# Performance work log

Hardware: AMD Instinct MI355X
Metric: run time of the kernel (lower is better)

The kernel has to match this reference:

```python
import jax, jax.numpy as jnp
import numpy as np

GRID_SIZE = 5
SPLINE_ORDER = 3
GRID_RANGE = (-1.0, 1.0)


def _make_grid():
    # knots: arange(-k, G+k+1)*h + lo, shared across in_features (uniform grid)
    h = (GRID_RANGE[1] - GRID_RANGE[0]) / GRID_SIZE
    return (jnp.arange(-SPLINE_ORDER, GRID_SIZE + SPLINE_ORDER + 1, dtype=jnp.float32) * h
            + GRID_RANGE[0])  # (G + 2k + 1,) = (12,)


def _b_splines(x2d, grid):
    # x2d: (T, C); grid: (12,) broadcast over features
    x = x2d[..., None]  # (T, C, 1)
    g = grid[None, None, :]  # (1, 1, 12)
    bases = ((x >= g[..., :-1]) & (x < g[..., 1:])).astype(x2d.dtype)
    for k in range(1, SPLINE_ORDER + 1):
        left = (x - g[..., : -(k + 1)]) / (g[..., k:-1] - g[..., : -(k + 1)])
        right = (g[..., k + 1:] - x) / (g[..., k + 1:] - g[..., 1:-k])
        bases = left * bases[..., :-1] + right * bases[..., 1:]
    return bases  # (T, C, G + k) = (T, C, 8)


def setup_inputs() -> dict:
    key = jax.random.key(0)
    k1, k2, k3, k4 = jax.random.split(key, 4)
    B, N, C, O = 4, 4096, 768, 768
    n_coef = GRID_SIZE + SPLINE_ORDER  # 8
    x = jax.random.normal(k1, (B, N, C), dtype=jnp.float32) * 0.5
    base_weight = jax.random.normal(k2, (O, C), dtype=jnp.float32) * (1.0 / np.sqrt(C))
    spline_weight = jax.random.normal(k3, (O, C, n_coef), dtype=jnp.float32) * 0.1
    spline_scaler = jax.random.normal(k4, (O, C), dtype=jnp.float32) * (1.0 / np.sqrt(C))
    return {"x": x, "base_weight": base_weight, "spline_weight": spline_weight,
            "spline_scaler": spline_scaler}


def reference(x, base_weight, spline_weight, spline_scaler):
    B, N, C = x.shape
    x2d = x.reshape(B * N, C)
    grid = _make_grid()
    # base path: SiLU activation + linear
    base_out = jnp.einsum('tc,oc->to', jax.nn.silu(x2d), base_weight)
    # spline path: B-spline bases + scaled linear combination
    bases = _b_splines(x2d, grid)  # (T, C, 8)
    w = spline_weight * spline_scaler[..., None]  # (O, C, 8)
    spline_out = jnp.einsum('tcg,ocg->to', bases, w)
    out = (base_out + spline_out).reshape(B, N, -1)
    return out  # dropout with p=0.0 is identity
```

## Files before the change

### kernel.cpp

```cpp
#include <hip/hip_runtime.h>

typedef __attribute__((ext_vector_type(8)))  short  short8;
typedef __attribute__((ext_vector_type(16))) float  f32x16;
typedef __attribute__((ext_vector_type(4)))  float  flt4;
typedef __attribute__((ext_vector_type(4)))  unsigned int u32x4;
typedef __attribute__((ext_vector_type(2)))  unsigned int u32x2;

#define T_DIM 16384
#define C_DIM 768
#define O_DIM 768

#define CK2    16
#define CHUNKS 48
#define KSTEPS 9
#define NSG    432
#define K3     6912
#define LDA3   152
#define BM     64
#define BN     384
#define LDSBUF 19456
#define WT3_BYTES  ((size_t)NSG * 12288 * 2)

__device__ __forceinline__ unsigned short f2bf(float f) {
  unsigned u = __float_as_uint(f);
  return (unsigned short)((u + 0x7FFFu + ((u >> 16) & 1u)) >> 16);
}

__device__ __forceinline__ unsigned cvtpk(float lo, float hi) {
  unsigned r;
  asm("v_cvt_pk_bf16_f32 %0, %1, %2" : "=v"(r) : "v"(lo), "v"(hi));
  return r;
}

__global__ void kan_prep3(const float* __restrict__ bw, const float* __restrict__ sw,
                          const float* __restrict__ sc, unsigned short* __restrict__ wt) {
  int id = blockIdx.x * 256 + threadIdx.x;
  if (id >= O_DIM * C_DIM) return;
  int o = id / C_DIM;
  int c = id - o * C_DIM;
  float b = bw[id];
  float s = sc[id];
  const float* sp = sw + (size_t)id * 8;
  {
    int k = (c >> 4) * 144 + (c & 15);
    wt[(size_t)(k >> 4) * 12288 + o * 16 + (k & 15)] = f2bf(b);
  }
#pragma unroll
  for (int g = 0; g < 8; ++g) {
    int k = (c >> 4) * 144 + 16 + (c & 15) * 8 + g;
    wt[(size_t)(k >> 4) * 12288 + o * 16 + (k & 15)] = f2bf(sp[g] * s);
  }
}

__global__ __launch_bounds__(256, 2) void kan_gemm6(
    const float* __restrict__ x, const unsigned short* __restrict__ wt,
    float* __restrict__ out) {
  __shared__ short Alds[2 * BM * LDA3];

  const int tid  = threadIdx.x;
  const int lane = tid & 63;
  const int wn   = tid >> 6;
  const int l31  = lane & 31;
  const int lq   = lane >> 5;

  const int d  = blockIdx.x;
  const int yt = d & 1;
  const int xt = d >> 1;
  const int tBase = xt * BM;
  const int oBase = yt * BN + wn * 96;

  f32x16 acc[2][3];
#pragma unroll
  for (int a = 0; a < 2; ++a)
#pragma unroll
    for (int b = 0; b < 3; ++b)
#pragma unroll
      for (int r = 0; r < 16; ++r) acc[a][b][r] = 0.0f;

  const int sRow = tid >> 2;
  const int sSb  = tid & 3;
  const float* xrow = x + (size_t)(tBase + sRow) * C_DIM + sSb * 4;

  char* ldsB = (char*)Alds;
  const int wbase = sRow * 304;
  int rbyte[2];
#pragma unroll
  for (int mf = 0; mf < 2; ++mf)
    rbyte[mf] = (mf * 32 + l31) * 304 + lq * 16;

  flt4 xa = *(const flt4*)(xrow);
  float    su[4];
  unsigned sww[16];

  auto stage_j = [&](int j) {
    float xx  = xa[j];
    float ex  = __expf(-xx);
    float sig = __builtin_amdgcn_rcpf(1.0f + ex);
    su[j] = xx * sig;
    float u  = fmaf(xx, 2.5f, 5.5f);
    float fl = floorf(u);
    int   jj = (int)fl;
    float f  = u - fl;
    float f2 = f * f, f3 = f2 * f;
    float W0 = f3 * (1.0f / 6.0f);
    float om = 1.0f - f;
    float W3 = om * om * om * (1.0f / 6.0f);
    float W2 = 0.5f * f3 - f2 + (2.0f / 3.0f);
    float W1 = 1.0f - W0 - W2 - W3;
    unsigned V0 = cvtpk(W3, W2);
    unsigned V1 = cvtpk(W1, W0);
    unsigned A0 = V0 << 16;
    unsigned A1 = (V1 << 16) | (V0 >> 16);
    unsigned A2 = V1 >> 16;
    int  k = jj - 3;
    int  q = k >> 1;
    bool r = (k & 1) != 0;
    unsigned U0 = r ? A0 : V0;
    unsigned U1 = r ? A1 : V1;
    unsigned U2 = r ? A2 : 0u;
#pragma unroll
    for (int p = 0; p < 4; ++p)
      sww[4 * j + p] =
          (q == p) ? U0 : ((q == p - 1) ? U1 : ((q == p - 2) ? U2 : 0u));
  };

#define WRITE_ONE(WR, WOFF)                                             \
  {                                                                     \
    if ((WR) == 0) {                                                    \
      u32x2 t;                                                          \
      t.x = cvtpk(su[0], su[1]); t.y = cvtpk(su[2], su[3]);             \
      *(u32x2*)(ldsB + (WOFF) + wbase + sSb * 8) = t;                   \
    } else {                                                            \
      u32x4 t;                                                          \
      t.x = sww[4 * ((WR) - 1)];     t.y = sww[4 * ((WR) - 1) + 1];     \
      t.z = sww[4 * ((WR) - 1) + 2]; t.w = sww[4 * ((WR) - 1) + 3];     \
      *(u32x4*)(ldsB + (WOFF) + wbase + 32 + sSb * 64 + ((WR) - 1) * 16) = t; \
    }                                                                   \
  }

#pragma unroll
  for (int j = 0; j < 4; ++j) stage_j(j);
  WRITE_ONE(0, 0) WRITE_ONE(1, 0) WRITE_ONE(2, 0) WRITE_ONE(3, 0) WRITE_ONE(4, 0)
  xa = *(const flt4*)(xrow + CK2);

  const size_t lofs = (size_t)(oBase + l31) * 16 + lq * 8;
  short8 bb0[3], bb1[3], bb2[3];
  {
    const unsigned short* w0 = wt + lofs;
    bb0[0] = *(const short8*)(w0);
    bb0[1] = *(const short8*)(w0 + 512);
    bb0[2] = *(const short8*)(w0 + 1024);
    const unsigned short* w1 = wt + 12288 + lofs;
    bb1[0] = *(const short8*)(w1);
    bb1[1] = *(const short8*)(w1 + 512);
    bb1[2] = *(const short8*)(w1 + 1024);
    const unsigned short* w2 = wt + 24576 + lofs;
    bb2[0] = *(const short8*)(w2);
    bb2[1] = *(const short8*)(w2 + 512);
    bb2[2] = *(const short8*)(w2 + 1024);
  }
  __syncthreads();

#define LDSA(MF, KS) (*(const short8*)(ldsB + roff + rbyte[MF] + (KS) * 32))
#define MFMA(A, B, C) __builtin_amdgcn_mfma_f32_32x32x16_bf16((A), (B), (C), 0, 0, 0)

  short8 aa0[2], aa1[2];

#define KSTEP(KS, BB, AAC, AAN, DOREAD, SJ, WR, DOX, GUARD)              \
  {                                                                      \
    if (DOREAD) {                                                        \
      AAN[0] = LDSA(0, (KS) + 1);                                        \
      AAN[1] = LDSA(1, (KS) + 1);                                        \
    }                                                                    \
    __builtin_amdgcn_s_setprio(1);                                       \
    acc[0][0] = MFMA(AAC[0], BB[0], acc[0][0]);                          \
    acc[0][1] = MFMA(AAC[0], BB[1], acc[0][1]);                          \
    acc[0][2] = MFMA(AAC[0], BB[2], acc[0][2]);                          \
    acc[1][0] = MFMA(AAC[1], BB[0], acc[1][0]);                          \
    acc[1][1] = MFMA(AAC[1], BB[1], acc[1][1]);                          \
    acc[1][2] = MFMA(AAC[1], BB[2], acc[1][2]);                          \
    __builtin_amdgcn_s_setprio(0);                                       \
    if (!(GUARD) || (chBase + (KS) + 3 < NSG)) {                         \
      const unsigned short* wp =                                         \
          wt + (size_t)(chBase + (KS) + 3) * 12288 + lofs;               \
      BB[0] = *(const short8*)(wp);                                      \
      BB[1] = *(const short8*)(wp + 512);                                \
      BB[2] = *(const short8*)(wp + 1024);                               \
    }                                                                    \
    if ((WR) >= 0) WRITE_ONE(WR, woff)                                   \
    if ((SJ) >= 0) stage_j(SJ);                                          \
    if (DOX) xa = *(const flt4*)(xrow + (ch + 2) * CK2);                 \
  }

  for (int ch = 0; ch < CHUNKS - 1; ++ch) {
    const int chBase = ch * KSTEPS;
    const int roff   = (ch & 1) * LDSBUF;
    const int woff   = roff ^ LDSBUF;
    const bool dox   = (ch + 2 < CHUNKS);
    aa0[0] = LDSA(0, 0);
    aa0[1] = LDSA(1, 0);
    KSTEP(0, bb0, aa0, aa1, 1,  0, -1, false, 0)
    KSTEP(1, bb1, aa1, aa0, 1,  1, -1, false, 0)
    KSTEP(2, bb2, aa0, aa1, 1,  2, -1, false, 0)
    KSTEP(3, bb0, aa1, aa0, 1,  3, -1, false, 0)
    KSTEP(4, bb1, aa0, aa1, 1, -1,  0, dox,   0)
    KSTEP(5, bb2, aa1, aa0, 1, -1,  1, false, 0)
    KSTEP(6, bb0, aa0, aa1, 1, -1,  2, false, 0)
    KSTEP(7, bb1, aa1, aa0, 1, -1,  3, false, 0)
    KSTEP(8, bb2, aa0, aa1, 0, -1,  4, false, 0)
    __syncthreads();
  }
  {
    const int ch     = CHUNKS - 1;
    (void)ch;
    const int chBase = (CHUNKS - 1) * KSTEPS;
    const int roff   = ((CHUNKS - 1) & 1) * LDSBUF;
    const int woff   = 0;
    (void)woff;
    aa0[0] = LDSA(0, 0);
    aa0[1] = LDSA(1, 0);
    KSTEP(0, bb0, aa0, aa1, 1, -1, -1, false, 1)
    KSTEP(1, bb1, aa1, aa0, 1, -1, -1, false, 1)
    KSTEP(2, bb2, aa0, aa1, 1, -1, -1, false, 1)
    KSTEP(3, bb0, aa1, aa0, 1, -1, -1, false, 1)
    KSTEP(4, bb1, aa0, aa1, 1, -1, -1, false, 1)
    KSTEP(5, bb2, aa1, aa0, 1, -1, -1, false, 1)
    KSTEP(6, bb0, aa0, aa1, 1, -1, -1, false, 1)
    KSTEP(7, bb1, aa1, aa0, 1, -1, -1, false, 1)
    KSTEP(8, bb2, aa0, aa1, 0, -1, -1, false, 1)
  }

#undef KSTEP
#undef LDSA
#undef MFMA
#undef WRITE_ONE

#pragma unroll
  for (int mf = 0; mf < 2; ++mf) {
    int tRow0 = tBase + mf * 32 + 4 * lq;
#pragma unroll
    for (int nf = 0; nf < 3; ++nf) {
      int oCol = oBase + nf * 32 + l31;
#pragma unroll
      for (int r = 0; r < 16; ++r) {
        int rowf = (r & 3) + 8 * (r >> 2);
        out[(size_t)(tRow0 + rowf) * O_DIM + oCol] = acc[mf][nf][r];
      }
    }
  }
}

__global__ __launch_bounds__(256, 2) void kan_gemm_fb(
    const float* __restrict__ x, const float* __restrict__ bw,
    const float* __restrict__ sw, const float* __restrict__ sc,
    float* __restrict__ out) {
  __shared__ short Alds[128 * 152];
  const int tid  = threadIdx.x;
  const int lane = tid & 63;
  const int wave = tid >> 6;
  const int wm   = wave >> 1;
  const int wn   = wave & 1;
  const int l31  = lane & 31;
  const int lq   = lane >> 5;
  const int tBase = blockIdx.x * 128;
  const int oBase = blockIdx.y * 192 + wn * 96;
  f32x16 acc[2][3];
#pragma unroll
  for (int a = 0; a < 2; ++a)
#pragma unroll
    for (int b = 0; b < 3; ++b)
#pragma unroll
      for (int r = 0; r < 16; ++r) acc[a][b][r] = 0.0f;
  const int sRow = tid >> 1;
  const int sSb  = tid & 1;
  const float* xrow = x + (size_t)(tBase + sRow) * C_DIM + sSb * 8;
  for (int ch = 0; ch < 48; ++ch) {
    __syncthreads();
    const float* xp = xrow + ch * 16;
    flt4 xv0 = *(const flt4*)(xp);
    flt4 xv1 = *(const flt4*)(xp + 4);
    short8 plane[9];
#pragma unroll
    for (int j = 0; j < 8; ++j) {
      float xx  = (j < 4) ? xv0[j] : xv1[j - 4];
      float sig = 1.0f / (1.0f + __expf(-xx));
      plane[0][j] = f2bf(xx * sig);
      float u  = fmaf(xx, 2.5f, 5.5f);
      float fl = floorf(u);
      int   jj = (int)fl;
      float f  = u - fl;
      float f2 = f * f, f3 = f2 * f;
      float W0 = f3 * (1.0f / 6.0f);
      float om = 1.0f - f;
      float W3 = om * om * om * (1.0f / 6.0f);
      float W2 = 0.5f * f3 - f2 + (2.0f / 3.0f);
      float W1 = 1.0f - W0 - W2 - W3;
#pragma unroll
      for (int s = 0; s < 8; ++s) {
        int   dd  = jj - s;
        float v01 = (dd & 1) ? W1 : W0;
        float v23 = (dd & 1) ? W3 : W2;
        float v   = (dd & 2) ? v23 : v01;
        v = ((unsigned)dd < 4u) ? v : 0.0f;
        plane[1 + s][j] = f2bf(v);
      }
    }
    {
      short* arow = &Alds[sRow * 152 + sSb * 72];
#pragma unroll
      for (int g = 0; g < 9; ++g) *(short8*)(arow + g * 8) = plane[g];
    }
    __syncthreads();
    for (int ks = 0; ks < 9; ++ks) {
      const int sGlob = ch * 9 + ks;
      short8 bfr[3];
      const int h    = sGlob * 2 + lq;
      const int cblk = (h * 7282) >> 16;
      const int g    = h - cblk * 9;
      const int cb   = cblk * 8;
#pragma unroll
      for (int nf = 0; nf < 3; ++nf) {
        int col = oBase + nf * 32 + l31;
        const float* rowb = ((g == 0) ? bw : sc) + (size_t)col * C_DIM + cb;
        flt4 s0 = *(const flt4*)rowb;
        flt4 s1 = *(const flt4*)(rowb + 4);
        short8 v;
        if (g == 0) {
#pragma unroll
          for (int j = 0; j < 8; ++j) v[j] = f2bf((j < 4) ? s0[j] : s1[j - 4]);
        } else {
          const float* sp = sw + ((size_t)col * C_DIM + cb) * 8 + (g - 1);
#pragma unroll
          for (int j = 0; j < 8; ++j) {
            float scv = (j < 4) ? s0[j] : s1[j - 4];
            v[j] = f2bf(sp[j * 8] * scv);
          }
        }
        bfr[nf] = v;
      }
      short8 afr[2];
#pragma unroll
      for (int mf = 0; mf < 2; ++mf)
        afr[mf] = *(const short8*)&Alds[(wm * 64 + mf * 32 + l31) * 152 + ks * 16 + lq * 8];
#pragma unroll
      for (int mf = 0; mf < 2; ++mf)
#pragma unroll
        for (int nf = 0; nf < 3; ++nf)
          acc[mf][nf] = __builtin_amdgcn_mfma_f32_32x32x16_bf16(
              afr[mf], bfr[nf], acc[mf][nf], 0, 0, 0);
    }
  }
#pragma unroll
  for (int mf = 0; mf < 2; ++mf) {
    int tRow0 = tBase + wm * 64 + mf * 32 + 4 * lq;
#pragma unroll
    for (int nf = 0; nf < 3; ++nf) {
      int oCol = oBase + nf * 32 + l31;
#pragma unroll
      for (int r = 0; r < 16; ++r) {
        int rowf = (r & 3) + 8 * (r >> 2);
        out[(size_t)(tRow0 + rowf) * O_DIM + oCol] = acc[mf][nf][r];
      }
    }
  }
}

extern "C" void kernel_launch(void* const* d_in, const int* in_sizes, int n_in,
                              void* d_out, int out_size, void* d_ws, size_t ws_size,
                              hipStream_t stream) {
  const float* x  = (const float*)d_in[0];
  const float* bw = (const float*)d_in[1];
  const float* sw = (const float*)d_in[2];
  const float* sc = (const float*)d_in[3];
  float* out = (float*)d_out;

  const bool use_ws = (d_ws != nullptr) && (ws_size >= WT3_BYTES);
  if (use_ws) {
    unsigned short* wt = (unsigned short*)d_ws;
    kan_prep3<<<(O_DIM * C_DIM + 255) / 256, 256, 0, stream>>>(bw, sw, sc, wt);
    kan_gemm6<<<dim3((T_DIM / BM) * (O_DIM / BN)), 256, 0, stream>>>(x, wt, out);
  } else {
    kan_gemm_fb<<<dim3(T_DIM / 128, O_DIM / 192), 256, 0, stream>>>(x, bw, sw, sc, out);
  }
}
```

Measured before the change: 179.0 us.

## Widen GEMM block to full output width with 512 threads sharing A tile

The block tile now spans all 768 outputs and uses 512 threads (8 waves), so each block of 64 tokens computes the SiLU and B-spline A tile once instead of twice across two N-tiles. Staging work is split across twice as many threads, each handling 2 features instead of 4, and the pipeline schedule is rearranged to match. This removes the redundant activation and basis computation and the duplicate x reads. In exchange the grid is halved to 256 blocks, and the larger blocks may lower occupancy or cause register pressure under the 512-thread launch bound.

```diff
diff --git a/kernel.cpp b/kernel.cpp
--- a/kernel.cpp
+++ b/kernel.cpp
@@ -3,6 +3,7 @@
 typedef __attribute__((ext_vector_type(8)))  short  short8;
 typedef __attribute__((ext_vector_type(16))) float  f32x16;
 typedef __attribute__((ext_vector_type(4)))  float  flt4;
+typedef __attribute__((ext_vector_type(2)))  float  flt2;
 typedef __attribute__((ext_vector_type(4)))  unsigned int u32x4;
 typedef __attribute__((ext_vector_type(2)))  unsigned int u32x2;
 
@@ -17,7 +18,7 @@
 #define K3     6912
 #define LDA3   152
 #define BM     64
-#define BN     384
+#define BN     768
 #define LDSBUF 19456
 #define WT3_BYTES  ((size_t)NSG * 12288 * 2)
 
@@ -52,7 +53,7 @@
   }
 }
 
-__global__ __launch_bounds__(256, 2) void kan_gemm6(
+__global__ __launch_bounds__(512, 2) void kan_gemm8(
     const float* __restrict__ x, const unsigned short* __restrict__ wt,
     float* __restrict__ out) {
   __shared__ short Alds[2 * BM * LDA3];
@@ -64,10 +65,8 @@
   const int lq   = lane >> 5;
 
   const int d  = blockIdx.x;
-  const int yt = d & 1;
-  const int xt = d >> 1;
-  const int tBase = xt * BM;
-  const int oBase = yt * BN + wn * 96;
+  const int tBase = d * BM;
+  const int oBase = wn * 96;
 
   f32x16 acc[2][3];
 #pragma unroll
@@ -77,9 +76,9 @@
 #pragma unroll
       for (int r = 0; r < 16; ++r) acc[a][b][r] = 0.0f;
 
-  const int sRow = tid >> 2;
-  const int sSb  = tid & 3;
-  const float* xrow = x + (size_t)(tBase + sRow) * C_DIM + sSb * 4;
+  const int sRow = tid >> 3;
+  const int sSb  = tid & 7;
+  const float* xrow = x + (size_t)(tBase + sRow) * C_DIM + sSb * 2;
 
   char* ldsB = (char*)Alds;
   const int wbase = sRow * 304;
@@ -88,9 +87,9 @@
   for (int mf = 0; mf < 2; ++mf)
     rbyte[mf] = (mf * 32 + l31) * 304 + lq * 16;
 
-  flt4 xa = *(const flt4*)(xrow);
-  float    su[4];
-  unsigned sww[16];
+  flt2 xa = *(const flt2*)(xrow);
+  float    su[2];
+  unsigned sww[8];
 
   auto stage_j = [&](int j) {
     float xx  = xa[j];
@@ -127,21 +126,18 @@
 #define WRITE_ONE(WR, WOFF)                                             \
   {                                                                     \
     if ((WR) == 0) {                                                    \
-      u32x2 t;                                                          \
-      t.x = cvtpk(su[0], su[1]); t.y = cvtpk(su[2], su[3]);             \
-      *(u32x2*)(ldsB + (WOFF) + wbase + sSb * 8) = t;                   \
+      *(unsigned*)(ldsB + (WOFF) + wbase + sSb * 4) = cvtpk(su[0], su[1]); \
     } else {                                                            \
       u32x4 t;                                                          \
       t.x = sww[4 * ((WR) - 1)];     t.y = sww[4 * ((WR) - 1) + 1];     \
       t.z = sww[4 * ((WR) - 1) + 2]; t.w = sww[4 * ((WR) - 1) + 3];     \
-      *(u32x4*)(ldsB + (WOFF) + wbase + 32 + sSb * 64 + ((WR) - 1) * 16) = t; \
+      *(u32x4*)(ldsB + (WOFF) + wbase + 32 + sSb * 32 + ((WR) - 1) * 16) = t; \
     }                                                                   \
   }
 
-#pragma unroll
-  for (int j = 0; j < 4; ++j) stage_j(j);
-  WRITE_ONE(0, 0) WRITE_ONE(1, 0) WRITE_ONE(2, 0) WRITE_ONE(3, 0) WRITE_ONE(4, 0)
-  xa = *(const flt4*)(xrow + CK2);
+  stage_j(0); stage_j(1);
+  WRITE_ONE(0, 0) WRITE_ONE(1, 0) WRITE_ONE(2, 0)
+  xa = *(const flt2*)(xrow + CK2);
 
   const size_t lofs = (size_t)(oBase + l31) * 16 + lq * 8;
   short8 bb0[3], bb1[3], bb2[3];
@@ -189,7 +185,7 @@
     }                                                                    \
     if ((WR) >= 0) WRITE_ONE(WR, woff)                                   \
     if ((SJ) >= 0) stage_j(SJ);                                          \
-    if (DOX) xa = *(const flt4*)(xrow + (ch + 2) * CK2);                 \
+    if (DOX) xa = *(const flt2*)(xrow + (ch + 2) * CK2);                 \
   }
 
   for (int ch = 0; ch < CHUNKS - 1; ++ch) {
@@ -201,13 +197,13 @@
     aa0[1] = LDSA(1, 0);
     KSTEP(0, bb0, aa0, aa1, 1,  0, -1, false, 0)
     KSTEP(1, bb1, aa1, aa0, 1,  1, -1, false, 0)
-    KSTEP(2, bb2, aa0, aa1, 1,  2, -1, false, 0)
-    KSTEP(3, bb0, aa1, aa0, 1,  3, -1, false, 0)
-    KSTEP(4, bb1, aa0, aa1, 1, -1,  0, dox,   0)
+    KSTEP(2, bb2, aa0, aa1, 1, -1, -1, dox,   0)
+    KSTEP(3, bb0, aa1, aa0, 1, -1, -1, false, 0)
+    KSTEP(4, bb1, aa0, aa1, 1, -1,  0, false, 0)
     KSTEP(5, bb2, aa1, aa0, 1, -1,  1, false, 0)
     KSTEP(6, bb0, aa0, aa1, 1, -1,  2, false, 0)
-    KSTEP(7, bb1, aa1, aa0, 1, -1,  3, false, 0)
-    KSTEP(8, bb2, aa0, aa1, 0, -1,  4, false, 0)
+    KSTEP(7, bb1, aa1, aa0, 1, -1, -1, false, 0)
+    KSTEP(8, bb2, aa0, aa1, 0, -1, -1, false, 0)
     __syncthreads();
   }
   {
@@ -378,7 +374,7 @@
   if (use_ws) {
     unsigned short* wt = (unsigned short*)d_ws;
     kan_prep3<<<(O_DIM * C_DIM + 255) / 256, 256, 0, stream>>>(bw, sw, sc, wt);
-    kan_gemm6<<<dim3((T_DIM / BM) * (O_DIM / BN)), 256, 0, stream>>>(x, wt, out);
+    kan_gemm8<<<dim3(T_DIM / BM), 512, 0, stream>>>(x, wt, out);
   } else {
     kan_gemm_fb<<<dim3(T_DIM / 128, O_DIM / 192), 256, 0, stream>>>(x, bw, sw, sc, out);
   }
```

New measurement: 166.9 us. -6.8%, faster.

## Widen GEMM tile to full output width with 8 waves and split A staging

Applied to the files above, without the earlier changes.

The fused KAN GEMM now uses 512-thread blocks, each covering a 64-row tile across all 768 output columns. Before, two blocks per row tile each recomputed the SiLU and B-spline expansion of the same activations. The two 4-wave groups take alternate 16-column chunks of x to stage into a 4-buffer LDS ring, and the loop processes two chunks per barrier. This removes the duplicated activation staging and halves the number of barriers, at the cost of double the LDS per block, larger blocks that may reduce occupancy, and fewer blocks (256) to fill the device.

```diff
diff --git a/kernel.cpp b/kernel.cpp
--- a/kernel.cpp
+++ b/kernel.cpp
@@ -14,10 +14,9 @@
 #define CHUNKS 48
 #define KSTEPS 9
 #define NSG    432
-#define K3     6912
 #define LDA3   152
 #define BM     64
-#define BN     384
+#define BN     768
 #define LDSBUF 19456
 #define WT3_BYTES  ((size_t)NSG * 12288 * 2)
 
@@ -52,22 +51,21 @@
   }
 }
 
-__global__ __launch_bounds__(256, 2) void kan_gemm6(
+__global__ __launch_bounds__(512, 2) void kan_gemm11(
     const float* __restrict__ x, const unsigned short* __restrict__ wt,
     float* __restrict__ out) {
-  __shared__ short Alds[2 * BM * LDA3];
+  __shared__ short Alds[4 * BM * LDA3];
 
   const int tid  = threadIdx.x;
   const int lane = tid & 63;
-  const int wn   = tid >> 6;
+  const int wave = tid >> 6;
   const int l31  = lane & 31;
   const int lq   = lane >> 5;
+  const bool wA  = (wave < 4);
 
   const int d  = blockIdx.x;
-  const int yt = d & 1;
-  const int xt = d >> 1;
-  const int tBase = xt * BM;
-  const int oBase = yt * BN + wn * 96;
+  const int tBase = d * BM;
+  const int oBase = wave * 96;
 
   f32x16 acc[2][3];
 #pragma unroll
@@ -77,8 +75,10 @@
 #pragma unroll
       for (int r = 0; r < 16; ++r) acc[a][b][r] = 0.0f;
 
-  const int sRow = tid >> 2;
-  const int sSb  = tid & 3;
+  const int tl   = tid & 255;
+  const int sRow = tl >> 2;
+  const int sSb  = tl & 3;
+  const int grpOff = wA ? 0 : 1;
   const float* xrow = x + (size_t)(tBase + sRow) * C_DIM + sSb * 4;
 
   char* ldsB = (char*)Alds;
@@ -88,7 +88,7 @@
   for (int mf = 0; mf < 2; ++mf)
     rbyte[mf] = (mf * 32 + l31) * 304 + lq * 16;
 
-  flt4 xa = *(const flt4*)(xrow);
+  flt4 xa;
   float    su[4];
   unsigned sww[16];
 
@@ -138,10 +138,20 @@
     }                                                                   \
   }
 
-#pragma unroll
-  for (int j = 0; j < 4; ++j) stage_j(j);
-  WRITE_ONE(0, 0) WRITE_ONE(1, 0) WRITE_ONE(2, 0) WRITE_ONE(3, 0) WRITE_ONE(4, 0)
-  xa = *(const flt4*)(xrow + CK2);
+#define SOP(I)                                                          \
+  {                                                                     \
+    if ((I) < 4)      stage_j(I);                                       \
+    else if ((I) < 9) WRITE_ONE((I) - 4, wo)                            \
+    else              { if (nc < CHUNKS) xa = *(const flt4*)(xrow + nc * CK2); } \
+  }
+
+  xa = *(const flt4*)(xrow + grpOff * CK2);
+  stage_j(0); stage_j(1); stage_j(2); stage_j(3);
+  {
+    const int wo = grpOff * LDSBUF;
+    WRITE_ONE(0, wo) WRITE_ONE(1, wo) WRITE_ONE(2, wo) WRITE_ONE(3, wo) WRITE_ONE(4, wo)
+  }
+  xa = *(const flt4*)(xrow + (2 + grpOff) * CK2);
 
   const size_t lofs = (size_t)(oBase + l31) * 16 + lq * 8;
   short8 bb0[3], bb1[3], bb2[3];
@@ -161,16 +171,16 @@
   }
   __syncthreads();
 
-#define LDSA(MF, KS) (*(const short8*)(ldsB + roff + rbyte[MF] + (KS) * 32))
+#define LDSA2(MF, KS, ROF) (*(const short8*)(ldsB + (ROF) + rbyte[MF] + (KS) * 32))
 #define MFMA(A, B, C) __builtin_amdgcn_mfma_f32_32x32x16_bf16((A), (B), (C), 0, 0, 0)
 
   short8 aa0[2], aa1[2];
 
-#define KSTEP(KS, BB, AAC, AAN, DOREAD, SJ, WR, DOX, GUARD)              \
+#define KSTEP(S, BB, AAC, AAN, DOREAD, ROFN, GUARD, STG)                 \
   {                                                                      \
     if (DOREAD) {                                                        \
-      AAN[0] = LDSA(0, (KS) + 1);                                        \
-      AAN[1] = LDSA(1, (KS) + 1);                                        \
+      AAN[0] = LDSA2(0, ((S) + 1) % 9, ROFN);                            \
+      AAN[1] = LDSA2(1, ((S) + 1) % 9, ROFN);                            \
     }                                                                    \
     __builtin_amdgcn_s_setprio(1);                                       \
     acc[0][0] = MFMA(AAC[0], BB[0], acc[0][0]);                          \
@@ -180,59 +190,79 @@
     acc[1][1] = MFMA(AAC[1], BB[1], acc[1][1]);                          \
     acc[1][2] = MFMA(AAC[1], BB[2], acc[1][2]);                          \
     __builtin_amdgcn_s_setprio(0);                                       \
-    if (!(GUARD) || (chBase + (KS) + 3 < NSG)) {                         \
+    if (!(GUARD) || (sgB + (S) + 3 < NSG)) {                             \
       const unsigned short* wp =                                         \
-          wt + (size_t)(chBase + (KS) + 3) * 12288 + lofs;               \
+          wt + (size_t)(sgB + (S) + 3) * 12288 + lofs;                   \
       BB[0] = *(const short8*)(wp);                                      \
       BB[1] = *(const short8*)(wp + 512);                                \
       BB[2] = *(const short8*)(wp + 1024);                               \
     }                                                                    \
-    if ((WR) >= 0) WRITE_ONE(WR, woff)                                   \
-    if ((SJ) >= 0) stage_j(SJ);                                          \
-    if (DOX) xa = *(const flt4*)(xrow + (ch + 2) * CK2);                 \
-  }
-
-  for (int ch = 0; ch < CHUNKS - 1; ++ch) {
-    const int chBase = ch * KSTEPS;
-    const int roff   = (ch & 1) * LDSBUF;
-    const int woff   = roff ^ LDSBUF;
-    const bool dox   = (ch + 2 < CHUNKS);
-    aa0[0] = LDSA(0, 0);
-    aa0[1] = LDSA(1, 0);
-    KSTEP(0, bb0, aa0, aa1, 1,  0, -1, false, 0)
-    KSTEP(1, bb1, aa1, aa0, 1,  1, -1, false, 0)
-    KSTEP(2, bb2, aa0, aa1, 1,  2, -1, false, 0)
-    KSTEP(3, bb0, aa1, aa0, 1,  3, -1, false, 0)
-    KSTEP(4, bb1, aa0, aa1, 1, -1,  0, dox,   0)
-    KSTEP(5, bb2, aa1, aa0, 1, -1,  1, false, 0)
-    KSTEP(6, bb0, aa0, aa1, 1, -1,  2, false, 0)
-    KSTEP(7, bb1, aa1, aa0, 1, -1,  3, false, 0)
-    KSTEP(8, bb2, aa0, aa1, 0, -1,  4, false, 0)
+    if (STG) {                                                           \
+      if ((S) <= 9 && wA)   SOP(S)                                       \
+      if ((S) >= 8 && !wA)  SOP((S) - 8)                                 \
+    }                                                                    \
+  }
+
+  for (int p = 0; p < 23; ++p) {
+    const int sgB   = p * 18;
+    const int roffA = ((2 * p) & 3) * LDSBUF;
+    const int roffB = ((2 * p + 1) & 3) * LDSBUF;
+    const int wo    = ((2 * p + 2 + grpOff) & 3) * LDSBUF;
+    const int nc    = 2 * p + 4 + grpOff;
+    aa0[0] = LDSA2(0, 0, roffA);
+    aa0[1] = LDSA2(1, 0, roffA);
+    KSTEP( 0, bb0, aa0, aa1, 1, roffA, 0, 1)
+    KSTEP( 1, bb1, aa1, aa0, 1, roffA, 0, 1)
+    KSTEP( 2, bb2, aa0, aa1, 1, roffA, 0, 1)
+    KSTEP( 3, bb0, aa1, aa0, 1, roffA, 0, 1)
+    KSTEP( 4, bb1, aa0, aa1, 1, roffA, 0, 1)
+    KSTEP( 5, bb2, aa1, aa0, 1, roffA, 0, 1)
+    KSTEP( 6, bb0, aa0, aa1, 1, roffA, 0, 1)
+    KSTEP( 7, bb1, aa1, aa0, 1, roffA, 0, 1)
+    KSTEP( 8, bb2, aa0, aa1, 1, roffB, 0, 1)
+    KSTEP( 9, bb0, aa1, aa0, 1, roffB, 0, 1)
+    KSTEP(10, bb1, aa0, aa1, 1, roffB, 0, 1)
+    KSTEP(11, bb2, aa1, aa0, 1, roffB, 0, 1)
+    KSTEP(12, bb0, aa0, aa1, 1, roffB, 0, 1)
+    KSTEP(13, bb1, aa1, aa0, 1, roffB, 0, 1)
+    KSTEP(14, bb2, aa0, aa1, 1, roffB, 0, 1)
+    KSTEP(15, bb0, aa1, aa0, 1, roffB, 0, 1)
+    KSTEP(16, bb1, aa0, aa1, 1, roffB, 0, 1)
+    KSTEP(17, bb2, aa1, aa0, 0, roffB, 0, 1)
     __syncthreads();
   }
   {
-    const int ch     = CHUNKS - 1;
-    (void)ch;
-    const int chBase = (CHUNKS - 1) * KSTEPS;
-    const int roff   = ((CHUNKS - 1) & 1) * LDSBUF;
-    const int woff   = 0;
-    (void)woff;
-    aa0[0] = LDSA(0, 0);
-    aa0[1] = LDSA(1, 0);
-    KSTEP(0, bb0, aa0, aa1, 1, -1, -1, false, 1)
-    KSTEP(1, bb1, aa1, aa0, 1, -1, -1, false, 1)
-    KSTEP(2, bb2, aa0, aa1, 1, -1, -1, false, 1)
-    KSTEP(3, bb0, aa1, aa0, 1, -1, -1, false, 1)
-    KSTEP(4, bb1, aa0, aa1, 1, -1, -1, false, 1)
-    KSTEP(5, bb2, aa1, aa0, 1, -1, -1, false, 1)
-    KSTEP(6, bb0, aa0, aa1, 1, -1, -1, false, 1)
-    KSTEP(7, bb1, aa1, aa0, 1, -1, -1, false, 1)
-    KSTEP(8, bb2, aa0, aa1, 0, -1, -1, false, 1)
+    const int sgB   = 23 * 18;
+    const int roffA = (46 & 3) * LDSBUF;
+    const int roffB = (47 & 3) * LDSBUF;
+    const int wo    = 0; (void)wo;
+    const int nc    = CHUNKS; (void)nc;
+    aa0[0] = LDSA2(0, 0, roffA);
+    aa0[1] = LDSA2(1, 0, roffA);
+    KSTEP( 0, bb0, aa0, aa1, 1, roffA, 1, 0)
+    KSTEP( 1, bb1, aa1, aa0, 1, roffA, 1, 0)
+    KSTEP( 2, bb2, aa0, aa1, 1, roffA, 1, 0)
+    KSTEP( 3, bb0, aa1, aa0, 1, roffA, 1, 0)
+    KSTEP( 4, bb1, aa0, aa1, 1, roffA, 1, 0)
+    KSTEP( 5, bb2, aa1, aa0, 1, roffA, 1, 0)
+    KSTEP( 6, bb0, aa0, aa1, 1, roffA, 1, 0)
+    KSTEP( 7, bb1, aa1, aa0, 1, roffA, 1, 0)
+    KSTEP( 8, bb2, aa0, aa1, 1, roffB, 1, 0)
+    KSTEP( 9, bb0, aa1, aa0, 1, roffB, 1, 0)
+    KSTEP(10, bb1, aa0, aa1, 1, roffB, 1, 0)
+    KSTEP(11, bb2, aa1, aa0, 1, roffB, 1, 0)
+    KSTEP(12, bb0, aa0, aa1, 1, roffB, 1, 0)
+    KSTEP(13, bb1, aa1, aa0, 1, roffB, 1, 0)
+    KSTEP(14, bb2, aa0, aa1, 1, roffB, 1, 0)
+    KSTEP(15, bb0, aa1, aa0, 1, roffB, 1, 0)
+    KSTEP(16, bb1, aa0, aa1, 1, roffB, 1, 0)
+    KSTEP(17, bb2, aa1, aa0, 0, roffB, 1, 0)
   }
 
 #undef KSTEP
-#undef LDSA
+#undef LDSA2
 #undef MFMA
+#undef SOP
 #undef WRITE_ONE
 
 #pragma unroll
@@ -378,7 +408,7 @@
   if (use_ws) {
     unsigned short* wt = (unsigned short*)d_ws;
     kan_prep3<<<(O_DIM * C_DIM + 255) / 256, 256, 0, stream>>>(bw, sw, sc, wt);
-    kan_gemm6<<<dim3((T_DIM / BM) * (O_DIM / BN)), 256, 0, stream>>>(x, wt, out);
+    kan_gemm11<<<dim3(T_DIM / BM), 512, 0, stream>>>(x, wt, out);
   } else {
     kan_gemm_fb<<<dim3(T_DIM / 128, O_DIM / 192), 256, 0, stream>>>(x, bw, sw, sc, out);
   }
```

Measured after the change: 172.9 us. 1.04x faster.
